# Performance work log

Measured on AMD Instinct MI355X. Metric: run time of the kernel, lower is better.

The kernel has to match this reference:

```python
import jax, jax.numpy as jnp
import numpy as np

INPUT_SIZE = 20
HIDDEN = 51
OUT = 1
B = 4096
T = 512


def _init_lstm_params(key, in_dim, hid_dim):
    # PyTorch LSTMCell init: U(-1/sqrt(hid), 1/sqrt(hid))
    k = 1.0 / np.sqrt(hid_dim)
    ks = jax.random.split(key, 4)
    W_ih = jax.random.uniform(ks[0], (4 * hid_dim, in_dim), minval=-k, maxval=k, dtype=jnp.float32)
    W_hh = jax.random.uniform(ks[1], (4 * hid_dim, hid_dim), minval=-k, maxval=k, dtype=jnp.float32)
    b_ih = jax.random.uniform(ks[2], (4 * hid_dim,), minval=-k, maxval=k, dtype=jnp.float32)
    b_hh = jax.random.uniform(ks[3], (4 * hid_dim,), minval=-k, maxval=k, dtype=jnp.float32)
    return W_ih, W_hh, b_ih, b_hh


def setup_inputs() -> dict:
    key = jax.random.key(0)
    k_x, k1, k2, k3, k4 = jax.random.split(key, 5)
    x = jax.random.normal(k_x, (B, T, INPUT_SIZE), dtype=jnp.float32)
    W_ih1, W_hh1, b_ih1, b_hh1 = _init_lstm_params(k1, INPUT_SIZE, HIDDEN)
    W_ih2, W_hh2, b_ih2, b_hh2 = _init_lstm_params(k2, HIDDEN, OUT)
    kl = 1.0 / np.sqrt(OUT)
    ka, kb, kc, kd = jax.random.split(k3, 4)
    W_mu = jax.random.uniform(ka, (OUT, OUT), minval=-kl, maxval=kl, dtype=jnp.float32)
    b_mu = jax.random.uniform(kb, (OUT,), minval=-kl, maxval=kl, dtype=jnp.float32)
    W_lv = jax.random.uniform(kc, (OUT, OUT), minval=-kl, maxval=kl, dtype=jnp.float32)
    b_lv = jax.random.uniform(kd, (OUT,), minval=-kl, maxval=kl, dtype=jnp.float32)
    return {
        "x": x,
        "W_ih1": W_ih1, "W_hh1": W_hh1, "b_ih1": b_ih1, "b_hh1": b_hh1,
        "W_ih2": W_ih2, "W_hh2": W_hh2, "b_ih2": b_ih2, "b_hh2": b_hh2,
        "W_mu": W_mu, "b_mu": b_mu, "W_lv": W_lv, "b_lv": b_lv,
    }


def _lstm_cell(x_t, h, c, W_ih, W_hh, b_ih, b_hh):
    # PyTorch LSTMCell: gate order i, f, g, o
    gates = x_t @ W_ih.T + b_ih + h @ W_hh.T + b_hh
    i, f, g, o = jnp.split(gates, 4, axis=-1)
    c_new = jax.nn.sigmoid(f) * c + jax.nn.sigmoid(i) * jnp.tanh(g)
    h_new = jax.nn.sigmoid(o) * jnp.tanh(c_new)
    return h_new, c_new


def reference(x, W_ih1, W_hh1, b_ih1, b_hh1, W_ih2, W_hh2, b_ih2, b_hh2, W_mu, b_mu, W_lv, b_lv):
    bsz = x.shape[0]
    h1 = jnp.zeros((bsz, HIDDEN), dtype=x.dtype)
    c1 = jnp.zeros((bsz, HIDDEN), dtype=x.dtype)
    h2 = jnp.zeros((bsz, OUT), dtype=x.dtype)
    c2 = jnp.zeros((bsz, OUT), dtype=x.dtype)

    def step(carry, x_t):
        h1, c1, h2, c2 = carry
        h1, c1 = _lstm_cell(x_t, h1, c1, W_ih1, W_hh1, b_ih1, b_hh1)
        h2, c2 = _lstm_cell(h1, h2, c2, W_ih2, W_hh2, b_ih2, b_hh2)
        return (h1, c1, h2, c2), h2

    xs = jnp.swapaxes(x, 0, 1)  # [T, B, input_size]
    _, h2_seq = jax.lax.scan(step, (h1, c1, h2, c2), xs)  # h2_seq: [T, B, 1]
    agg = jnp.mean(h2_seq, axis=0)  # [B, 1] mean over time
    mu = agg @ W_mu.T + b_mu
    log_var = agg @ W_lv.T + b_lv
    sigma = jnp.exp(0.5 * log_var)
    lower = mu - 1.96 * sigma
    upper = mu + 1.96 * sigma
    return (lower, mu, upper, log_var)
```

## Files before the change

### kernel.cpp

```cpp
#include <hip/hip_runtime.h>

#define B_TOT 4096
#define T_STEPS 512
#define IN 20
#define HID 51

typedef float f32x4 __attribute__((ext_vector_type(4)));
typedef short s16x8 __attribute__((ext_vector_type(8)));

__device__ __forceinline__ unsigned short f2bf(float f) {
    unsigned int u = __float_as_uint(f);
    unsigned int r = (u + 0x7fffu + ((u >> 16) & 1u)) >> 16;
    return (unsigned short)r;
}

#define L2E  1.4426950408889634f
#define L2E2 2.8853900817779268f

__device__ __forceinline__ float fast_rcp(float x) { return __builtin_amdgcn_rcpf(x); }
__device__ __forceinline__ float ex2(float x)      { return __builtin_amdgcn_exp2f(x); }
__device__ __forceinline__ float sig_p(float p)  { return fast_rcp(1.0f + ex2(p)); }
__device__ __forceinline__ float tanh_q(float q) { return 1.0f - 2.0f * fast_rcp(1.0f + ex2(q)); }
__device__ __forceinline__ float tanh2_q(float q) {
    return __builtin_fmaf(fast_rcp(1.0f + ex2(q)), -2.0f * L2E2, L2E2);
}


__global__ __launch_bounds__(896)
void lstm_fused(const float* __restrict__ x,
                const float* __restrict__ Wih1, const float* __restrict__ Whh1,
                const float* __restrict__ bih1, const float* __restrict__ bhh1,
                const float* __restrict__ Wih2, const float* __restrict__ Whh2,
                const float* __restrict__ bih2, const float* __restrict__ bhh2,
                const float* __restrict__ Wmu,  const float* __restrict__ bmu,
                const float* __restrict__ Wlv,  const float* __restrict__ blv,
                float* __restrict__ out)
{
    __shared__ __align__(16) unsigned short vA[2][2][64][8];
    __shared__ __align__(16) unsigned short xS[4][64][8];

    const int tid  = threadIdx.x;
    const int lane = tid & 63;
    const int w    = tid >> 6;
    const int bidx = blockIdx.x;

    const int  tile  = (w == 2) ? 12 : (w == 12) ? 2 : w;
    const bool isT   = (w <= 12);
    const bool isFAT = (w == 2);
    const bool isST  = (w == 13);

    s16x8 wfrag[3];
    f32x4 binit = {0.f, 0.f, 0.f, 0.f};
    {
        const int m = lane & 15;
        #pragma unroll
        for (int ks = 0; ks < 3; ++ks) {
            s16x8 f;
            #pragma unroll
            for (int j = 0; j < 8; ++j) {
                int k = ks * 32 + ((lane >> 4) << 3) + j;
                float v = 0.0f;
                if (isT) {
                    if (isFAT && m >= 12) {
                        int g2 = m - 12;
                        if (k >= 32 && k < 32 + HID)
                            v = Wih2[g2 * HID + (k - 32)] * ((g2 == 2) ? L2E2 : -L2E);
                    } else {
                        int g = m & 3, unit = tile * 4 + (m >> 2);
                        if (unit < HID) {
                            int row = g * HID + unit;
                            if (k < IN) v = Wih1[row * IN + k];
                            else if (k >= 32 && k < 32 + HID) v = Whh1[row * HID + (k - 32)];
                            v *= (g == 2) ? L2E2 : -L2E;
                        }
                    }
                }
                f[j] = (short)f2bf(v);
            }
            wfrag[ks] = f;
        }
        if (isT) {
            if (isFAT && (lane >> 4) == 3) {
                #pragma unroll
                for (int r = 0; r < 4; ++r)
                    binit[r] = (bih2[r] + bhh2[r]) * ((r == 2) ? L2E2 : -L2E);
            } else {
                int unit = tile * 4 + (lane >> 4);
                if (unit < HID) {
                    #pragma unroll
                    for (int r = 0; r < 4; ++r)
                        binit[r] = (bih1[r * HID + unit] + bhh1[r * HID + unit]) * ((r == 2) ? L2E2 : -L2E);
                }
            }
        }
    }

    float whh2g[4] = {0.f, 0.f, 0.f, 0.f};
    if (isFAT) {
        #pragma unroll
        for (int r = 0; r < 4; ++r) whh2g[r] = Whh2[r] * ((r == 2) ? L2E2 : -L2E);
    }

    int hchunk = 0, hrow = 0, hj = 0;
    if (isT) {
        int unit = tile * 4 + (lane >> 4);
        int k    = 32 + unit;
        hchunk = (k >> 5) - 1;
        hrow   = (((k >> 3) & 3) << 4) + (lane & 15);
        hj     = k & 7;
    }

    const float* sp[5];
    int srow[5], sj[5];
    if (isST) {
        #pragma unroll
        for (int i = 0; i < 5; ++i) {
            int e = i * 64 + lane;
            int b = e / IN, m = e % IN;
            sp[i]   = x + ((size_t)(bidx * 16 + b) * T_STEPS) * IN + m;
            srow[i] = ((m >> 3) & 3) * 16 + b;
            sj[i]   = m & 7;
        }
    }

    {
        unsigned short* vz = &vA[0][0][0][0];
        for (int i = tid; i < 2 * 2 * 64 * 8; i += 896) vz[i] = 0;
        unsigned short* xz = &xS[0][0][0];
        for (int i = tid; i < 4 * 64 * 8; i += 896) xz[i] = 0;
    }
    __syncthreads();
    float rE[5], rO[5];
    if (isST) {
        #pragma unroll
        for (int i = 0; i < 5; ++i) {
            xS[0][srow[i]][sj[i]] = f2bf(sp[i][0]);
            xS[1][srow[i]][sj[i]] = f2bf(sp[i][IN]);
            rE[i] = sp[i][(size_t)2 * IN];
            rO[i] = sp[i][(size_t)3 * IN];
        }
    }
    __syncthreads();

    f32x4 accx = {0.f, 0.f, 0.f, 0.f};
    if (isT) {
        const s16x8 b00 = *(const s16x8*)&xS[0][lane][0];
        accx = __builtin_amdgcn_mfma_f32_16x16x32_bf16(wfrag[0], b00, binit, 0, 0, 0);
    }

    float C1t = 0.f;
    float C2p = 0.f, h2p = 0.f, sum2 = 0.f;
    f32x4 aP = {0.f, 0.f, 0.f, 0.f};

#define STEP(tt, P, XR, XW, XREG)                                                \
    {                                                                            \
        if (isST) {                                                              \
            const int t4 = ((tt) < T_STEPS - 4) ? (tt) + 4 : T_STEPS - 1;        \
            _Pragma("unroll")                                                    \
            for (int i = 0; i < 5; ++i) {                                        \
                xS[XW][srow[i]][sj[i]] = f2bf(XREG[i]);                          \
                XREG[i] = sp[i][(size_t)t4 * IN];                                \
            }                                                                    \
        }                                                                        \
        if (isT) {                                                               \
            const s16x8 bf1  = *(const s16x8*)&vA[P][0][lane][0];                \
            const s16x8 bf2  = *(const s16x8*)&vA[P][1][lane][0];                \
            const s16x8 bf0n = *(const s16x8*)&xS[XR][lane][0];                  \
              \
            if (isFAT && (tt) >= 2 && lane >= 48) {                              \
                float pi = aP[0] + whh2g[0] * h2p;                               \
                float pf = aP[1] + whh2g[1] * h2p;                               \
                float pg = aP[2] + whh2g[2] * h2p;                               \
                float po = aP[3] + whh2g[3] * h2p;                               \
                float C2 = sig_p(pf) * C2p + sig_p(pi) * tanh2_q(pg);            \
                C2p = C2;                                                        \
                h2p = sig_p(po) * tanh_q(C2);                                    \
                sum2 += h2p;                                                     \
            }                                                                    \
            f32x4 a = accx;                                                      \
            a = __builtin_amdgcn_mfma_f32_16x16x32_bf16(wfrag[1], bf1, a, 0, 0, 0); \
            a = __builtin_amdgcn_mfma_f32_16x16x32_bf16(wfrag[2], bf2, a, 0, 0, 0); \
            if (isFAT) aP = a;                                                   \
                                        \
            float ei = ex2(a[0]), ef = ex2(a[1]), eg = ex2(a[2]), eo = ex2(a[3]);\
            float Pi = 1.f + ei, Pf = 1.f + ef, Pg = 1.f + eg, Po = 1.f + eo;    \
            float Pig = Pi * Pg;                                                 \
            float rr  = fast_rcp(Pf * Pig);                                      \
            float C   = __builtin_fmaf(C1t, Pig, L2E2 * ((eg - 1.f) * Pf)) * rr; \
            C1t = C;                                                             \
            float ec  = ex2(fminf(C, 126.f));                                    \
            float h   = (ec - 1.f) * fast_rcp(Po * (1.f + ec));                  \
            if (!(isFAT && (lane >> 4) == 3))                                    \
                vA[(P) ^ 1][hchunk][hrow][hj] = f2bf(h);                         \
            accx = __builtin_amdgcn_mfma_f32_16x16x32_bf16(wfrag[0], bf0n, binit, 0, 0, 0); \
        }                                                                        \
        __syncthreads();                                                         \
    }

    for (int t = 0; t < T_STEPS; t += 4) {
        STEP(t + 0, 0, 1, 2, rE)
        STEP(t + 1, 1, 2, 3, rO)
        STEP(t + 2, 0, 3, 0, rE)
        STEP(t + 3, 1, 0, 1, rO)
    }
#undef STEP

    if (isFAT) {
        if (lane >= 48) {
            float pi = aP[0] + whh2g[0] * h2p;
            float pf = aP[1] + whh2g[1] * h2p;
            float pg = aP[2] + whh2g[2] * h2p;
            float po = aP[3] + whh2g[3] * h2p;
            float C2 = sig_p(pf) * C2p + sig_p(pi) * tanh2_q(pg);
            C2p = C2;
            h2p = sig_p(po) * tanh_q(C2);
            sum2 += h2p;
        }
        const s16x8 bf1 = *(const s16x8*)&vA[0][0][lane][0];
        const s16x8 bf2 = *(const s16x8*)&vA[0][1][lane][0];
        f32x4 a = accx;
        a = __builtin_amdgcn_mfma_f32_16x16x32_bf16(wfrag[1], bf1, a, 0, 0, 0);
        a = __builtin_amdgcn_mfma_f32_16x16x32_bf16(wfrag[2], bf2, a, 0, 0, 0);
        if (lane >= 48) {
            float pi = a[0] + whh2g[0] * h2p;
            float pf = a[1] + whh2g[1] * h2p;
            float pg = a[2] + whh2g[2] * h2p;
            float po = a[3] + whh2g[3] * h2p;
            float C2 = sig_p(pf) * C2p + sig_p(pi) * tanh2_q(pg);
            h2p = sig_p(po) * tanh_q(C2);
            sum2 += h2p;

            float agg = sum2 * (1.0f / 512.0f);
            float mu  = Wmu[0] * agg + bmu[0];
            float lv  = Wlv[0] * agg + blv[0];
            float sg  = __expf(0.5f * lv);
            int bg = bidx * 16 + (lane & 15);
            out[bg]             = mu - 1.96f * sg;
            out[B_TOT + bg]     = mu;
            out[2 * B_TOT + bg] = mu + 1.96f * sg;
            out[3 * B_TOT + bg] = lv;
        }
    }
}

extern "C" void kernel_launch(void* const* d_in, const int* in_sizes, int n_in,
                              void* d_out, int out_size, void* d_ws, size_t ws_size,
                              hipStream_t stream) {
    const float* x    = (const float*)d_in[0];
    const float* Wih1 = (const float*)d_in[1];
    const float* Whh1 = (const float*)d_in[2];
    const float* bih1 = (const float*)d_in[3];
    const float* bhh1 = (const float*)d_in[4];
    const float* Wih2 = (const float*)d_in[5];
    const float* Whh2 = (const float*)d_in[6];
    const float* bih2 = (const float*)d_in[7];
    const float* bhh2 = (const float*)d_in[8];
    const float* Wmu  = (const float*)d_in[9];
    const float* bmu  = (const float*)d_in[10];
    const float* Wlv  = (const float*)d_in[11];
    const float* blv  = (const float*)d_in[12];
    float* out = (float*)d_out;

    lstm_fused<<<dim3(B_TOT / 16), dim3(896), 0, stream>>>(
        x, Wih1, Whh1, bih1, bhh1, Wih2, Whh2, bih2, bhh2, Wmu, bmu, Wlv, blv, out);
}
```

Before: 431.2 us.

## Load x directly into MFMA B-fragments per wave, dropping staging wave and LDS buffer

Removes the dedicated staging wave and its LDS ring for x. Each compute wave now loads its own x slice straight from global memory into registers two steps ahead and packs it into bf16 MFMA fragments with v_cvt_pk_bf16_f32. The block shrinks from 14 to 13 waves, which cuts LDS traffic and barrier participants. In exchange every compute wave issues its own global loads with a shorter prefetch distance, and the same x data is loaded redundantly across the 13 waves.

```diff
diff --git a/kernel.cpp b/kernel.cpp
--- a/kernel.cpp
+++ b/kernel.cpp
@@ -12,6 +12,12 @@
     unsigned int u = __float_as_uint(f);
     unsigned int r = (u + 0x7fffu + ((u >> 16) & 1u)) >> 16;
     return (unsigned short)r;
+}
+
+__device__ __forceinline__ unsigned int cvtpk(float a, float b) {
+    unsigned int d;
+    asm("v_cvt_pk_bf16_f32 %0, %1, %2" : "=v"(d) : "v"(a), "v"(b));
+    return d;
 }
 
 #define L2E  1.4426950408889634f
@@ -26,7 +32,7 @@
 }
 
 
-__global__ __launch_bounds__(896)
+__global__ __launch_bounds__(832)
 void lstm_fused(const float* __restrict__ x,
                 const float* __restrict__ Wih1, const float* __restrict__ Whh1,
                 const float* __restrict__ bih1, const float* __restrict__ bhh1,
@@ -37,7 +43,6 @@
                 float* __restrict__ out)
 {
     __shared__ __align__(16) unsigned short vA[2][2][64][8];
-    __shared__ __align__(16) unsigned short xS[4][64][8];
 
     const int tid  = threadIdx.x;
     const int lane = tid & 63;
@@ -45,9 +50,7 @@
     const int bidx = blockIdx.x;
 
     const int  tile  = (w == 2) ? 12 : (w == 12) ? 2 : w;
-    const bool isT   = (w <= 12);
     const bool isFAT = (w == 2);
-    const bool isST  = (w == 13);
 
     s16x8 wfrag[3];
     f32x4 binit = {0.f, 0.f, 0.f, 0.f};
@@ -60,37 +63,33 @@
             for (int j = 0; j < 8; ++j) {
                 int k = ks * 32 + ((lane >> 4) << 3) + j;
                 float v = 0.0f;
-                if (isT) {
-                    if (isFAT && m >= 12) {
-                        int g2 = m - 12;
-                        if (k >= 32 && k < 32 + HID)
-                            v = Wih2[g2 * HID + (k - 32)] * ((g2 == 2) ? L2E2 : -L2E);
-                    } else {
-                        int g = m & 3, unit = tile * 4 + (m >> 2);
-                        if (unit < HID) {
-                            int row = g * HID + unit;
-                            if (k < IN) v = Wih1[row * IN + k];
-                            else if (k >= 32 && k < 32 + HID) v = Whh1[row * HID + (k - 32)];
-                            v *= (g == 2) ? L2E2 : -L2E;
-                        }
+                if (isFAT && m >= 12) {
+                    int g2 = m - 12;
+                    if (k >= 32 && k < 32 + HID)
+                        v = Wih2[g2 * HID + (k - 32)] * ((g2 == 2) ? L2E2 : -L2E);
+                } else {
+                    int g = m & 3, unit = tile * 4 + (m >> 2);
+                    if (unit < HID) {
+                        int row = g * HID + unit;
+                        if (k < IN) v = Wih1[row * IN + k];
+                        else if (k >= 32 && k < 32 + HID) v = Whh1[row * HID + (k - 32)];
+                        v *= (g == 2) ? L2E2 : -L2E;
                     }
                 }
                 f[j] = (short)f2bf(v);
             }
             wfrag[ks] = f;
         }
-        if (isT) {
-            if (isFAT && (lane >> 4) == 3) {
+        if (isFAT && (lane >> 4) == 3) {
+            #pragma unroll
+            for (int r = 0; r < 4; ++r)
+                binit[r] = (bih2[r] + bhh2[r]) * ((r == 2) ? L2E2 : -L2E);
+        } else {
+            int unit = tile * 4 + (lane >> 4);
+            if (unit < HID) {
                 #pragma unroll
                 for (int r = 0; r < 4; ++r)
-                    binit[r] = (bih2[r] + bhh2[r]) * ((r == 2) ? L2E2 : -L2E);
-            } else {
-                int unit = tile * 4 + (lane >> 4);
-                if (unit < HID) {
-                    #pragma unroll
-                    for (int r = 0; r < 4; ++r)
-                        binit[r] = (bih1[r * HID + unit] + bhh1[r * HID + unit]) * ((r == 2) ? L2E2 : -L2E);
-                }
+                    binit[r] = (bih1[r * HID + unit] + bhh1[r * HID + unit]) * ((r == 2) ? L2E2 : -L2E);
             }
         }
     }
@@ -101,8 +100,8 @@
         for (int r = 0; r < 4; ++r) whh2g[r] = Whh2[r] * ((r == 2) ? L2E2 : -L2E);
     }
 
-    int hchunk = 0, hrow = 0, hj = 0;
-    if (isT) {
+    int hchunk, hrow, hj;
+    {
         int unit = tile * 4 + (lane >> 4);
         int k    = 32 + unit;
         hchunk = (k >> 5) - 1;
@@ -110,98 +109,84 @@
         hj     = k & 7;
     }
 
-    const float* sp[5];
-    int srow[5], sj[5];
-    if (isST) {
-        #pragma unroll
-        for (int i = 0; i < 5; ++i) {
-            int e = i * 64 + lane;
-            int b = e / IN, m = e % IN;
-            sp[i]   = x + ((size_t)(bidx * 16 + b) * T_STEPS) * IN + m;
-            srow[i] = ((m >> 3) & 3) * 16 + b;
-            sj[i]   = m & 7;
-        }
-    }
+    const int  k0  = (lane >> 4) << 3;
+    const bool ldv = (lane < 48);
+    const bool ldh = (lane < 32);
+    const float* xb = x + ((size_t)(bidx * 16 + (lane & 15)) * T_STEPS) * IN + k0;
 
     {
         unsigned short* vz = &vA[0][0][0][0];
-        for (int i = tid; i < 2 * 2 * 64 * 8; i += 896) vz[i] = 0;
-        unsigned short* xz = &xS[0][0][0];
-        for (int i = tid; i < 4 * 64 * 8; i += 896) xz[i] = 0;
+        for (int i = tid; i < 2 * 2 * 64 * 8; i += 832) vz[i] = 0;
     }
     __syncthreads();
-    float rE[5], rO[5];
-    if (isST) {
-        #pragma unroll
-        for (int i = 0; i < 5; ++i) {
-            xS[0][srow[i]][sj[i]] = f2bf(sp[i][0]);
-            xS[1][srow[i]][sj[i]] = f2bf(sp[i][IN]);
-            rE[i] = sp[i][(size_t)2 * IN];
-            rO[i] = sp[i][(size_t)3 * IN];
-        }
-    }
-    __syncthreads();
-
-    f32x4 accx = {0.f, 0.f, 0.f, 0.f};
-    if (isT) {
-        const s16x8 b00 = *(const s16x8*)&xS[0][lane][0];
-        accx = __builtin_amdgcn_mfma_f32_16x16x32_bf16(wfrag[0], b00, binit, 0, 0, 0);
+
+    const f32x4 zero4 = {0.f, 0.f, 0.f, 0.f};
+    f32x4 loE = zero4, hiE = zero4, loO = zero4, hiO = zero4;
+    if (ldv) loE = *(const f32x4*)(xb);
+    if (ldh) hiE = *(const f32x4*)(xb + 4);
+    if (ldv) loO = *(const f32x4*)(xb + IN);
+    if (ldh) hiO = *(const f32x4*)(xb + IN + 4);
+
+    union frag_u { s16x8 f; unsigned int u[4]; };
+    f32x4 accx;
+    {
+        frag_u fb;
+        fb.u[0] = cvtpk(loE[0], loE[1]); fb.u[1] = cvtpk(loE[2], loE[3]);
+        fb.u[2] = cvtpk(hiE[0], hiE[1]); fb.u[3] = cvtpk(hiE[2], hiE[3]);
+        accx = __builtin_amdgcn_mfma_f32_16x16x32_bf16(wfrag[0], fb.f, binit, 0, 0, 0);
     }
 
     float C1t = 0.f;
     float C2p = 0.f, h2p = 0.f, sum2 = 0.f;
     f32x4 aP = {0.f, 0.f, 0.f, 0.f};
 
-#define STEP(tt, P, XR, XW, XREG)                                                \
+#define STEP(tt, P, loA, hiA, loB, hiB)                                          \
     {                                                                            \
-        if (isST) {                                                              \
-            const int t4 = ((tt) < T_STEPS - 4) ? (tt) + 4 : T_STEPS - 1;        \
-            _Pragma("unroll")                                                    \
-            for (int i = 0; i < 5; ++i) {                                        \
-                xS[XW][srow[i]][sj[i]] = f2bf(XREG[i]);                          \
-                XREG[i] = sp[i][(size_t)t4 * IN];                                \
-            }                                                                    \
+        const int t2 = ((tt) < T_STEPS - 2) ? (tt) + 2 : T_STEPS - 1;            \
+        const float* p = xb + (size_t)t2 * IN;                                   \
+        if (ldv) loA = *(const f32x4*)p;                                         \
+        if (ldh) hiA = *(const f32x4*)(p + 4);                                   \
+        const s16x8 bf1 = *(const s16x8*)&vA[P][0][lane][0];                     \
+        const s16x8 bf2 = *(const s16x8*)&vA[P][1][lane][0];                     \
+              \
+        if (isFAT && (tt) >= 2 && lane >= 48) {                                  \
+            float pi = aP[0] + whh2g[0] * h2p;                                   \
+            float pf = aP[1] + whh2g[1] * h2p;                                   \
+            float pg = aP[2] + whh2g[2] * h2p;                                   \
+            float po = aP[3] + whh2g[3] * h2p;                                   \
+            float C2 = sig_p(pf) * C2p + sig_p(pi) * tanh2_q(pg);                \
+            C2p = C2;                                                            \
+            h2p = sig_p(po) * tanh_q(C2);                                        \
+            sum2 += h2p;                                                         \
         }                                                                        \
-        if (isT) {                                                               \
-            const s16x8 bf1  = *(const s16x8*)&vA[P][0][lane][0];                \
-            const s16x8 bf2  = *(const s16x8*)&vA[P][1][lane][0];                \
-            const s16x8 bf0n = *(const s16x8*)&xS[XR][lane][0];                  \
-              \
-            if (isFAT && (tt) >= 2 && lane >= 48) {                              \
-                float pi = aP[0] + whh2g[0] * h2p;                               \
-                float pf = aP[1] + whh2g[1] * h2p;                               \
-                float pg = aP[2] + whh2g[2] * h2p;                               \
-                float po = aP[3] + whh2g[3] * h2p;                               \
-                float C2 = sig_p(pf) * C2p + sig_p(pi) * tanh2_q(pg);            \
-                C2p = C2;                                                        \
-                h2p = sig_p(po) * tanh_q(C2);                                    \
-                sum2 += h2p;                                                     \
-            }                                                                    \
-            f32x4 a = accx;                                                      \
-            a = __builtin_amdgcn_mfma_f32_16x16x32_bf16(wfrag[1], bf1, a, 0, 0, 0); \
-            a = __builtin_amdgcn_mfma_f32_16x16x32_bf16(wfrag[2], bf2, a, 0, 0, 0); \
-            if (isFAT) aP = a;                                                   \
+        f32x4 a = accx;                                                          \
+        a = __builtin_amdgcn_mfma_f32_16x16x32_bf16(wfrag[1], bf1, a, 0, 0, 0);  \
+        a = __builtin_amdgcn_mfma_f32_16x16x32_bf16(wfrag[2], bf2, a, 0, 0, 0);  \
+        if (isFAT) aP = a;                                                       \
                                         \
-            float ei = ex2(a[0]), ef = ex2(a[1]), eg = ex2(a[2]), eo = ex2(a[3]);\
-            float Pi = 1.f + ei, Pf = 1.f + ef, Pg = 1.f + eg, Po = 1.f + eo;    \
-            float Pig = Pi * Pg;                                                 \
-            float rr  = fast_rcp(Pf * Pig);                                      \
-            float C   = __builtin_fmaf(C1t, Pig, L2E2 * ((eg - 1.f) * Pf)) * rr; \
-            C1t = C;                                                             \
-            float ec  = ex2(fminf(C, 126.f));                                    \
-            float h   = (ec - 1.f) * fast_rcp(Po * (1.f + ec));                  \
-            if (!(isFAT && (lane >> 4) == 3))                                    \
-                vA[(P) ^ 1][hchunk][hrow][hj] = f2bf(h);                         \
-            accx = __builtin_amdgcn_mfma_f32_16x16x32_bf16(wfrag[0], bf0n, binit, 0, 0, 0); \
+        float ei = ex2(a[0]), ef = ex2(a[1]), eg = ex2(a[2]), eo = ex2(a[3]);    \
+        float Pi = 1.f + ei, Pf = 1.f + ef, Pg = 1.f + eg, Po = 1.f + eo;        \
+        float Pig = Pi * Pg;                                                     \
+        float rr  = fast_rcp(Pf * Pig);                                          \
+        float C   = __builtin_fmaf(C1t, Pig, L2E2 * ((eg - 1.f) * Pf)) * rr;     \
+        C1t = C;                                                                 \
+        float ec  = ex2(fminf(C, 126.f));                                        \
+        float h   = (ec - 1.f) * fast_rcp(Po * (1.f + ec));                      \
+        if (!(isFAT && (lane >> 4) == 3))                                        \
+            vA[(P) ^ 1][hchunk][hrow][hj] = (unsigned short)cvtpk(h, h);         \
+                     \
+        {                                                                        \
+            frag_u fb;                                                           \
+            fb.u[0] = cvtpk(loB[0], loB[1]); fb.u[1] = cvtpk(loB[2], loB[3]);    \
+            fb.u[2] = cvtpk(hiB[0], hiB[1]); fb.u[3] = cvtpk(hiB[2], hiB[3]);    \
+            accx = __builtin_amdgcn_mfma_f32_16x16x32_bf16(wfrag[0], fb.f, binit, 0, 0, 0); \
         }                                                                        \
         __syncthreads();                                                         \
     }
 
-    for (int t = 0; t < T_STEPS; t += 4) {
-        STEP(t + 0, 0, 1, 2, rE)
-        STEP(t + 1, 1, 2, 3, rO)
-        STEP(t + 2, 0, 3, 0, rE)
-        STEP(t + 3, 1, 0, 1, rO)
+    for (int t = 0; t < T_STEPS; t += 2) {
+        STEP(t + 0, 0, loE, hiE, loO, hiO)
+        STEP(t + 1, 1, loO, hiO, loE, hiE)
     }
 #undef STEP
 
@@ -261,6 +246,6 @@
     const float* blv  = (const float*)d_in[12];
     float* out = (float*)d_out;
 
-    lstm_fused<<<dim3(B_TOT / 16), dim3(896), 0, stream>>>(
+    lstm_fused<<<dim3(B_TOT / 16), dim3(832), 0, stream>>>(
         x, Wih1, Whh1, bih1, bhh1, Wih2, Whh2, bih2, bhh2, Wmu, bmu, Wlv, blv, out);
 }
```

Result: slower. 594.2 us (+37.8%).
